# Kernel tuning notes

Measured on AMD Instinct MI355X. Metric: run time of the kernel, lower is better.

## Reference

```python
import jax, jax.numpy as jnp
import numpy as np

# Window-batch of 16x16 windows from a U-Net stage
B, C, H, W = 128, 128, 16, 16
HEADS = 8
EQK, EV = 128, 512      # embed_dim_qk, embed_dim_v (embed_dim=512, ratio=4)
L = H * W               # tokens per window (stride=1)


def _conv3x3(x, w, b):
    # NCHW 3x3 conv, padding 1
    out = jax.lax.conv_general_dilated(x, w, (1, 1), ((1, 1), (1, 1)),
                                       dimension_numbers=('NCHW', 'OIHW', 'NCHW'))
    return out + b[None, :, None, None]


def _pos_att(q, wq, bq, wk, bk, wv, bv, wo, bo, gamma):
    # MultiHeadAttention2D_POS, stride=1 -> conv_q/k/v are 1x1 convs
    hd, hdv = EQK // HEADS, EV // HEADS

    def proj(x, w, bias, d):
        y = jnp.einsum('bchw,ec->behw', x, w) + bias[None, :, None, None]
        return y.reshape(B, HEADS, d, L).transpose(0, 1, 3, 2)  # (B,h,L,d)

    pq = proj(q, wq, bq, hd)
    pk = proj(q, wk, bk, hd)
    pv = proj(q, wv, bv, hdv)
    attn = jax.nn.softmax(jnp.einsum('bhqd,bhkd->bhqk', pq, pk) * hd ** -0.5, axis=-1)
    out = jnp.einsum('bhqk,bhkd->bhqd', attn, pv)
    out = out.transpose(0, 1, 3, 2).reshape(B, EV, H, W)
    out = _conv3x3(out, wo, bo)             # proj_out: 3x3 conv EV->C
    return q + out * gamma                  # gamma-scaled residual


def _cha_att(q, wq, bq, wk, bk, wv, bv, wo, bo, gamma):
    # MultiHeadAttention2D_CHA: depthwise 1x1 grouped convs (channel multiplier = HEADS),
    # attention over the CHANNEL axis. Faithfully reproduces torch's reshape of the
    # group-major (c*HEADS+h) channel layout into (B, heads, C, L).
    def dwproj(x, w, bias):
        y = (x[:, :, None] * w.reshape(C, HEADS)[None, :, :, None, None]
             + bias.reshape(C, HEADS)[None, :, :, None, None])
        return y.reshape(B, C * HEADS, H, W).reshape(B, HEADS, C, L)

    pq = dwproj(q, wq, bq)
    pk = dwproj(q, wk, bk)
    pv = dwproj(q, wv, bv)
    attn = jax.nn.softmax(jnp.einsum('bhcl,bhdl->bhcd', pq, pk) * L ** -0.5, axis=-1)
    out = jnp.einsum('bhcd,bhdl->bhcl', attn, pv)      # (B,h,C,L)
    out = out.reshape(B, HEADS * C, H, W)
    # proj_out: grouped 1x1 ConvTranspose (== grouped 1x1 conv): sum each HEADS-sized group
    out = (out.reshape(B, C, HEADS, H, W)
           * wo.reshape(C, HEADS)[None, :, :, None, None]).sum(2) + bo[None, :, None, None]
    return q + out * gamma


def _forward(qkv_pos, qkv_cha,
             pos_wq, pos_bq, pos_wk, pos_bk, pos_wv, pos_bv, pos_wo, pos_bo, gamma_pos,
             cha_wq, cha_bq, cha_wk, cha_bk, cha_wv, cha_bv, cha_wo, cha_bo, gamma_cha,
             fuse_w, fuse_b):
    out_pos = _pos_att(qkv_pos, pos_wq, pos_bq, pos_wk, pos_bk, pos_wv, pos_bv,
                       pos_wo, pos_bo, gamma_pos)
    out_cha = _cha_att(qkv_cha, cha_wq, cha_bq, cha_wk, cha_bk, cha_wv, cha_bv,
                       cha_wo, cha_bo, gamma_cha)
    out = (out_pos + out_cha) * 0.5          # att_fusion='add' (slides=0 -> full slices)
    return _conv3x3(out, fuse_w, fuse_b)     # conv_out (Dropout2d is identity at eval)


def setup_inputs() -> dict:
    key = jax.random.key(0)
    ks = jax.random.split(key, 24)
    n = lambda k, shape, s=0.05: jax.random.normal(k, shape, dtype=jnp.float32) * s
    return {
        'qkv_pos': jax.random.normal(ks[0], (B, C, H, W), jnp.float32),
        'qkv_cha': jax.random.normal(ks[1], (B, C, H, W), jnp.float32),
        'pos_wq': n(ks[2], (EQK, C)), 'pos_bq': n(ks[3], (EQK,)),
        'pos_wk': n(ks[4], (EQK, C)), 'pos_bk': n(ks[5], (EQK,)),
        'pos_wv': n(ks[6], (EV, C)), 'pos_bv': n(ks[7], (EV,)),
        'pos_wo': n(ks[8], (C, EV, 3, 3)), 'pos_bo': n(ks[9], (C,)),
        'gamma_pos': jnp.array(0.1, jnp.float32),
        'cha_wq': n(ks[10], (C * HEADS,)), 'cha_bq': n(ks[11], (C * HEADS,)),
        'cha_wk': n(ks[12], (C * HEADS,)), 'cha_bk': n(ks[13], (C * HEADS,)),
        'cha_wv': n(ks[14], (C * HEADS,)), 'cha_bv': n(ks[15], (C * HEADS,)),
        'cha_wo': n(ks[16], (C * HEADS,)), 'cha_bo': n(ks[17], (C,)),
        'gamma_cha': jnp.array(0.1, jnp.float32),
        'fuse_w': n(ks[18], (C, C, 3, 3)), 'fuse_b': n(ks[19], (C,)),
    }


def reference(qkv_pos, qkv_cha,
              pos_wq, pos_bq, pos_wk, pos_bk, pos_wv, pos_bv, pos_wo, pos_bo, gamma_pos,
              cha_wq, cha_bq, cha_wk, cha_bk, cha_wv, cha_bv, cha_wo, cha_bo, gamma_cha,
              fuse_w, fuse_b):
    return _forward(qkv_pos, qkv_cha,
                    pos_wq, pos_bq, pos_wk, pos_bk, pos_wv, pos_bv, pos_wo, pos_bo, gamma_pos,
                    cha_wq, cha_bq, cha_wk, cha_bk, cha_wv, cha_bv, cha_wo, cha_bo, gamma_cha,
                    fuse_w, fuse_b)
```

## Files before the change

### kernel.cpp

```cpp
#include <hip/hip_runtime.h>
#include <cstdint>
#include <cstddef>

typedef unsigned short ushort_t;
typedef unsigned int uint_t;
typedef __attribute__((ext_vector_type(8))) short bf16x8;
typedef __attribute__((ext_vector_type(4))) float f32x4;

#define NB 128
#define NC 128
#define NL 256
#define NH 8
#define HD 16
#define HDV 64
#define NEV 512
#define PHALF 4194304

__device__ __forceinline__ ushort_t f2bf(float f) {
    uint_t u = __float_as_uint(f);
    u += 0x7fffu + ((u >> 16) & 1u);
    return (ushort_t)(u >> 16);
}
__device__ __forceinline__ float bf2f(ushort_t s) {
    return __uint_as_float(((uint_t)s) << 16);
}
__device__ __forceinline__ uint_t pack2(float lo, float hi) {
    return ((uint_t)f2bf(hi) << 16) | (uint_t)f2bf(lo);
}

template<int CIN>
__global__ __launch_bounds__(256) void k_wpack(const float* __restrict__ w,
                                               short* __restrict__ wp) {
    int idx = blockIdx.x * 256 + threadIdx.x;
    if (idx >= CIN * 1152) return;
    int j    = idx & 7;
    int lane = (idx >> 3) & 63;
    int frag = idx >> 9;
    int rt   = frag & 7;
    int tap  = (frag >> 3) % 9;
    int ch   = frag / 72;
    int co   = rt * 16 + (lane & 15);
    int g    = lane >> 4;
    int ci   = ch * 32 + g * 8 + j;
    wp[idx] = (short)f2bf(w[((size_t)co * CIN + ci) * 9 + tap]);
}

template<int E>
__global__ __launch_bounds__(256) void k_wpack_qkv(const float* __restrict__ w,
                                                   short* __restrict__ wp) {
    int idx = blockIdx.x * 256 + threadIdx.x;
    if (idx >= E * 128) return;
    int j    = idx & 7;
    int lane = (idx >> 3) & 63;
    int ch   = (idx >> 9) & 3;
    int rt   = idx >> 11;
    int n = lane & 15, g = lane >> 4;
    wp[idx] = (short)f2bf(w[(size_t)(rt*16 + n)*128 + ch*32 + g*8 + j]);
}

__global__ __launch_bounds__(256) void k_pos_mfma(
    const float* __restrict__ x,
    const short* __restrict__ wpq, const short* __restrict__ wpk,
    const short* __restrict__ wpv,
    const float* __restrict__ bq, const float* __restrict__ bk,
    const float* __restrict__ bv,
    ushort_t* __restrict__ att)
{
    const int h = blockIdx.x, b = blockIdx.y;
    const int t = threadIdx.x;
    const int lane = t & 63, w = t >> 6;
    const int n = lane & 15, g = lane >> 4;

    __shared__ __align__(16) short lds[31232];

    const f32x4 z4 = {0.f, 0.f, 0.f, 0.f};
    f32x4 qacc[4], kacc[4], vacc[16];
    #pragma unroll
    for (int ct = 0; ct < 4; ++ct) { qacc[ct] = z4; kacc[ct] = z4; }
    #pragma unroll
    for (int i = 0; i < 16; ++i) vacc[i] = z4;

    const float* xg = x + (size_t)b * NC * NL + t;

    #pragma unroll 1
    for (int ch = 0; ch < 4; ++ch) {
        __syncthreads();
        #pragma unroll
        for (int k8 = 0; k8 < 4; ++k8) {
            bf16x8 v8;
            #pragma unroll
            for (int jj = 0; jj < 8; ++jj)
                v8[jj] = (short)f2bf(xg[(ch*32 + k8*8 + jj) * NL]);
            *(bf16x8*)&lds[t*40 + k8*8] = v8;
        }
        __syncthreads();
        bf16x8 xb[4];
        #pragma unroll
        for (int ct = 0; ct < 4; ++ct)
            xb[ct] = *(const bf16x8*)&lds[(w*64 + ct*16 + n)*40 + g*8];
        const size_t fo = ((size_t)((h*4 + ch)*64) + lane) * 8;
        {
            bf16x8 aq = *(const bf16x8*)(wpq + fo);
            #pragma unroll
            for (int ct = 0; ct < 4; ++ct)
                qacc[ct] = __builtin_amdgcn_mfma_f32_16x16x32_bf16(aq, xb[ct], qacc[ct], 0, 0, 0);
        }
        {
            bf16x8 ak = *(const bf16x8*)(wpk + fo);
            #pragma unroll
            for (int ct = 0; ct < 4; ++ct)
                kacc[ct] = __builtin_amdgcn_mfma_f32_16x16x32_bf16(ak, xb[ct], kacc[ct], 0, 0, 0);
        }
        #pragma unroll
        for (int vt = 0; vt < 4; ++vt) {
            bf16x8 av = *(const bf16x8*)(wpv + ((size_t)((((h*4 + vt)*4) + ch)*64) + lane) * 8);
            #pragma unroll
            for (int ct = 0; ct < 4; ++ct)
                vacc[vt*4+ct] = __builtin_amdgcn_mfma_f32_16x16x32_bf16(av, xb[ct], vacc[vt*4+ct], 0, 0, 0);
        }
    }
    __syncthreads();

    {
        float bqv[4], bkv[4];
        #pragma unroll
        for (int r = 0; r < 4; ++r) {
            bqv[r] = bq[h*16 + g*4 + r];
            bkv[r] = bk[h*16 + g*4 + r];
        }
        #pragma unroll
        for (int ct = 0; ct < 4; ++ct) {
            uint2 qp, kp;
            qp.x = pack2(qacc[ct][0] + bqv[0], qacc[ct][1] + bqv[1]);
            qp.y = pack2(qacc[ct][2] + bqv[2], qacc[ct][3] + bqv[3]);
            *(uint2*)&lds[w*1024 + (ct*16 + n)*16 + g*4] = qp;
            kp.x = pack2(kacc[ct][0] + bkv[0], kacc[ct][1] + bkv[1]);
            kp.y = pack2(kacc[ct][2] + bkv[2], kacc[ct][3] + bkv[3]);
            *(uint2*)&lds[10240 + (w*64 + ct*16 + n)*16 + g*4] = kp;
        }
        #pragma unroll
        for (int vt = 0; vt < 4; ++vt) {
            float bv0 = bv[h*64 + vt*16 + g*4 + 0];
            float bv1 = bv[h*64 + vt*16 + g*4 + 1];
            float bv2 = bv[h*64 + vt*16 + g*4 + 2];
            float bv3 = bv[h*64 + vt*16 + g*4 + 3];
            #pragma unroll
            for (int ct = 0; ct < 4; ++ct) {
                const int col = w*64 + ct*16 + n;
                lds[14336 + (vt*16 + g*4 + 0)*264 + col] = (short)f2bf(vacc[vt*4+ct][0] + bv0);
                lds[14336 + (vt*16 + g*4 + 1)*264 + col] = (short)f2bf(vacc[vt*4+ct][1] + bv1);
                lds[14336 + (vt*16 + g*4 + 2)*264 + col] = (short)f2bf(vacc[vt*4+ct][2] + bv2);
                lds[14336 + (vt*16 + g*4 + 3)*264 + col] = (short)f2bf(vacc[vt*4+ct][3] + bv3);
            }
        }
    }
    __syncthreads();

    #pragma unroll 1
    for (int qt = 0; qt < 4; ++qt) {
        bf16x8 qf = (bf16x8){0,0,0,0,0,0,0,0};
        if (g < 2) qf = *(const bf16x8*)&lds[w*1024 + (qt*16 + n)*16 + g*8];
        f32x4 s[16];
        #pragma unroll
        for (int kt = 0; kt < 16; ++kt) {
            bf16x8 kf = (bf16x8){0,0,0,0,0,0,0,0};
            if (g < 2) kf = *(const bf16x8*)&lds[10240 + (kt*16 + n)*16 + g*8];
            s[kt] = __builtin_amdgcn_mfma_f32_16x16x32_bf16(kf, qf, z4, 0, 0, 0);
        }
        float m = -3.0e38f;
        #pragma unroll
        for (int kt = 0; kt < 16; ++kt)
            #pragma unroll
            for (int r = 0; r < 4; ++r)
                m = fmaxf(m, s[kt][r]);
        m = fmaxf(m, __shfl_xor(m, 16));
        m = fmaxf(m, __shfl_xor(m, 32));
        float den = 0.f;
        #pragma unroll
        for (int kt = 0; kt < 16; ++kt)
            #pragma unroll
            for (int r = 0; r < 4; ++r) {
                float e = __expf((s[kt][r] - m) * 0.25f);
                s[kt][r] = e;
                den += e;
            }
        den += __shfl_xor(den, 16);
        den += __shfl_xor(den, 32);
        const float inv = 1.f / den;

        f32x4 oacc[4] = {z4, z4, z4, z4};
        #pragma unroll
        for (int c2 = 0; c2 < 8; ++c2) {
            #pragma unroll
            for (int u = 0; u < 2; ++u) {
                const int kt = 2*c2 + u;
                uint2 pp;
                pp.x = pack2(s[kt][0], s[kt][1]);
                pp.y = pack2(s[kt][2], s[kt][3]);
                *(uint2*)&lds[4096 + w*640 + n*40 + u*16 + g*4] = pp;
            }
            bf16x8 pf = *(const bf16x8*)&lds[4096 + w*640 + n*40 + g*8];
            #pragma unroll
            for (int vt = 0; vt < 4; ++vt) {
                bf16x8 av = *(const bf16x8*)&lds[14336 + (vt*16 + n)*264 + c2*32 + g*8];
                oacc[vt] = __builtin_amdgcn_mfma_f32_16x16x32_bf16(av, pf, oacc[vt], 0, 0, 0);
            }
        }
        ushort_t* ap = att + (((size_t)b*NL + (w*64 + qt*16 + n))*NEV + h*HDV + g*4);
        #pragma unroll
        for (int vt = 0; vt < 4; ++vt) {
            uint2 op;
            op.x = pack2(oacc[vt][0]*inv, oacc[vt][1]*inv);
            op.y = pack2(oacc[vt][2]*inv, oacc[vt][3]*inv);
            *(uint2*)(ap + vt*16) = op;
        }
    }
}

__global__ __launch_bounds__(512, 2) void k_conv_ci(
    const ushort_t* __restrict__ att, const short* __restrict__ wp,
    ushort_t* __restrict__ P)
{
    const int kc = blockIdx.x, b = blockIdx.y;
    const int t = threadIdx.x;
    const int lane = t & 63, w = t >> 6;
    const int wr = w >> 2, wc = w & 3;
    const int n = lane & 15, gl = lane >> 4;

    __shared__ __align__(16) short ims[2][10368];

    {
        bf16x8 z = {0,0,0,0,0,0,0,0};
        bf16x8* p = (bf16x8*)&ims[0][0];
        for (int i = t; i < 2592; i += 512) p[i] = z;
    }

    f32x4 acc[4][4];
    #pragma unroll
    for (int i = 0; i < 4; ++i)
        #pragma unroll
        for (int j = 0; j < 4; ++j) acc[i][j] = (f32x4){0.f,0.f,0.f,0.f};

    const int g1 = t & 3, x1 = (t >> 2) & 15, y1 = t >> 6;
    const ushort_t* src1 = att + ((size_t)(b*NL + y1*16 + x1))*NEV + kc*256 + g1*8;
    const ushort_t* src2 = att + ((size_t)(b*NL + (y1+8)*16 + x1))*NEV + kc*256 + g1*8;
    const int slot1 = (((y1+1)*4 + g1)*18 + x1 + 1) * 8;
    const int slot2 = (((y1+9)*4 + g1)*18 + x1 + 1) * 8;

    bf16x8 v1 = *(const bf16x8*)src1;
    bf16x8 v2 = *(const bf16x8*)src2;
    __syncthreads();

    #pragma unroll 1
    for (int ch = 0; ch < 8; ++ch) {
        short* buf = &ims[ch & 1][0];
        *(bf16x8*)&buf[slot1] = v1;
        *(bf16x8*)&buf[slot2] = v2;
        if (ch < 7) {
            v1 = *(const bf16x8*)(src1 + (ch + 1) * 32);
            v2 = *(const bf16x8*)(src2 + (ch + 1) * 32);
        }
        __syncthreads();
        #pragma unroll
        for (int tap = 0; tap < 9; ++tap) {
            const int dy = tap / 3, dx = tap % 3;
            bf16x8 Bf[4];
            #pragma unroll
            for (int ct = 0; ct < 4; ++ct)
                Bf[ct] = *(const bf16x8*)&buf[((((wc*4 + ct + dy)*4) + gl)*18 + n + dx) * 8];
            bf16x8 Af[4];
            #pragma unroll
            for (int rt = 0; rt < 4; ++rt)
                Af[rt] = *(const bf16x8*)(wp +
                    ((size_t)(((kc*8 + ch)*9 + tap)*8 + wr*4 + rt)) * 512 + lane*8);
            #pragma unroll
            for (int rt = 0; rt < 4; ++rt)
                #pragma unroll
                for (int ct = 0; ct < 4; ++ct)
                    acc[rt][ct] = __builtin_amdgcn_mfma_f32_16x16x32_bf16(
                        Af[rt], Bf[ct], acc[rt][ct], 0, 0, 0);
        }
    }

    ushort_t* Pb = P + (size_t)kc * PHALF + (size_t)b * NL * NC;
    #pragma unroll
    for (int rt = 0; rt < 4; ++rt) {
        const int co0 = wr*64 + rt*16 + gl*4;
        #pragma unroll
        for (int ct = 0; ct < 4; ++ct) {
            const int l = wc*64 + ct*16 + n;
            uint2 u;
            u.x = pack2(acc[rt][ct][0], acc[rt][ct][1]);
            u.y = pack2(acc[rt][ct][2], acc[rt][ct][3]);
            *(uint2*)(Pb + (size_t)l*NC + co0) = u;
        }
    }
}

__global__ __launch_bounds__(512, 2) void k_conv_co(
    const float* __restrict__ comb, const short* __restrict__ wp,
    const float* __restrict__ bias, float* __restrict__ out)
{
    const int kc = blockIdx.x, b = blockIdx.y;
    const int t = threadIdx.x;
    const int lane = t & 63, w = t >> 6;
    const int wr = w & 1, wc = w >> 1;
    const int n = lane & 15, gl = lane >> 4;

    __shared__ __align__(16) short ims[2][10368];

    {
        bf16x8 z = {0,0,0,0,0,0,0,0};
        bf16x8* p = (bf16x8*)&ims[0][0];
        for (int i = t; i < 2592; i += 512) p[i] = z;
    }

    f32x4 acc[2][4];
    #pragma unroll
    for (int i = 0; i < 2; ++i)
        #pragma unroll
        for (int j = 0; j < 4; ++j) acc[i][j] = (f32x4){0.f,0.f,0.f,0.f};

    const int g1 = t & 3, x1 = (t >> 2) & 15, y1 = t >> 6;
    const float* s1 = comb + ((size_t)(b*NL + y1*16 + x1))*NC + g1*8;
    const float* s2 = comb + ((size_t)(b*NL + (y1+8)*16 + x1))*NC + g1*8;
    const int slot1 = (((y1+1)*4 + g1)*18 + x1 + 1) * 8;
    const int slot2 = (((y1+9)*4 + g1)*18 + x1 + 1) * 8;

    float4 a1 = *(const float4*)s1,       b1_ = *(const float4*)(s1 + 4);
    float4 a2 = *(const float4*)s2,       b2_ = *(const float4*)(s2 + 4);
    __syncthreads();

    #pragma unroll 1
    for (int ch = 0; ch < 4; ++ch) {
        short* buf = &ims[ch & 1][0];
        bf16x8 w1, w2;
        w1[0]=(short)f2bf(a1.x);  w1[1]=(short)f2bf(a1.y);
        w1[2]=(short)f2bf(a1.z);  w1[3]=(short)f2bf(a1.w);
        w1[4]=(short)f2bf(b1_.x); w1[5]=(short)f2bf(b1_.y);
        w1[6]=(short)f2bf(b1_.z); w1[7]=(short)f2bf(b1_.w);
        w2[0]=(short)f2bf(a2.x);  w2[1]=(short)f2bf(a2.y);
        w2[2]=(short)f2bf(a2.z);  w2[3]=(short)f2bf(a2.w);
        w2[4]=(short)f2bf(b2_.x); w2[5]=(short)f2bf(b2_.y);
        w2[6]=(short)f2bf(b2_.z); w2[7]=(short)f2bf(b2_.w);
        *(bf16x8*)&buf[slot1] = w1;
        *(bf16x8*)&buf[slot2] = w2;
        if (ch < 3) {
            a1  = *(const float4*)(s1 + (ch+1)*32);
            b1_ = *(const float4*)(s1 + (ch+1)*32 + 4);
            a2  = *(const float4*)(s2 + (ch+1)*32);
            b2_ = *(const float4*)(s2 + (ch+1)*32 + 4);
        }
        __syncthreads();
        #pragma unroll
        for (int tap = 0; tap < 9; ++tap) {
            const int dy = tap / 3, dx = tap % 3;
            bf16x8 Bf[4];
            #pragma unroll
            for (int ct = 0; ct < 4; ++ct)
                Bf[ct] = *(const bf16x8*)&buf[((((wc*4 + ct + dy)*4) + gl)*18 + n + dx) * 8];
            bf16x8 Af[2];
            #pragma unroll
            for (int rt = 0; rt < 2; ++rt)
                Af[rt] = *(const bf16x8*)(wp +
                    ((size_t)((ch*9 + tap)*8 + kc*4 + wr*2 + rt)) * 512 + lane*8);
            #pragma unroll
            for (int rt = 0; rt < 2; ++rt)
                #pragma unroll
                for (int ct = 0; ct < 4; ++ct)
                    acc[rt][ct] = __builtin_amdgcn_mfma_f32_16x16x32_bf16(
                        Af[rt], Bf[ct], acc[rt][ct], 0, 0, 0);
        }
    }

    #pragma unroll
    for (int rt = 0; rt < 2; ++rt) {
        const int co0 = kc*64 + wr*32 + rt*16 + gl*4;
        const float c0 = bias[co0+0], c1 = bias[co0+1],
                    c2 = bias[co0+2], c3 = bias[co0+3];
        #pragma unroll
        for (int ct = 0; ct < 4; ++ct) {
            const int l = wc*64 + ct*16 + n;
            f32x4 a = acc[rt][ct];
            out[((size_t)b*NC + co0+0)*NL + l] = c0 + a[0];
            out[((size_t)b*NC + co0+1)*NL + l] = c1 + a[1];
            out[((size_t)b*NC + co0+2)*NL + l] = c2 + a[2];
            out[((size_t)b*NC + co0+3)*NL + l] = c3 + a[3];
        }
    }
}

#define NLP 260
__global__ __launch_bounds__(256) void k_cha(
    const float* __restrict__ xc,
    const float* __restrict__ cwq, const float* __restrict__ cbq,
    const float* __restrict__ cwk, const float* __restrict__ cbk,
    const float* __restrict__ cwv, const float* __restrict__ cbv,
    const float* __restrict__ cwo, const float* __restrict__ cbo,
    const float* __restrict__ gamma,
    const ushort_t* __restrict__ P, const float* __restrict__ qpos,
    const float* __restrict__ pbo, const float* __restrict__ gpos,
    float* __restrict__ comb)
{
    const int h = blockIdx.x, b = blockIdx.y, t = threadIdx.x;
    __shared__ float qh[16][NLP];
    __shared__ float G_s[16][17];
    __shared__ float S_s[16];
    __shared__ float wq_s[128], bq_s[128], wk_s[128], bk_s[128], wv_s[128], bv_s[128];
    __shared__ float A_s[128][17];
    __shared__ float B_s[128];
    __shared__ float M_s[16][17];
    __shared__ float c_s[16];

    #pragma unroll
    for (int j = 0; j < 16; ++j)
        qh[j][t] = xc[((size_t)b*NC + h*16 + j)*NL + t];
    if (t < 128) {
        const int k = h*128 + t;
        wq_s[t] = cwq[k]; bq_s[t] = cbq[k];
        wk_s[t] = cwk[k]; bk_s[t] = cbk[k];
        wv_s[t] = cwv[k]; bv_s[t] = cbv[k];
    }
    __syncthreads();
    {
        const int i = t >> 4, j = t & 15;
        const float4* qi = (const float4*)qh[i];
        const float4* qj = (const float4*)qh[j];
        float gg = 0.f;
        for (int l4 = 0; l4 < NL/4; ++l4) {
            float4 a = qi[l4], c = qj[l4];
            gg = fmaf(a.x,c.x,fmaf(a.y,c.y,fmaf(a.z,c.z,fmaf(a.w,c.w,gg))));
        }
        G_s[i][j] = gg;
    }
    if (t < 16) {
        const float4* qi = (const float4*)qh[t];
        float s = 0.f;
        for (int l4 = 0; l4 < NL/4; ++l4) { float4 a = qi[l4]; s += a.x + a.y + a.z + a.w; }
        S_s[t] = s;
    }
    __syncthreads();
    if (t < 128) {
        const int c2 = t, cg = c2 >> 3;
        const float wqc = wq_s[c2], bqc = bq_s[c2];
        float Pv[16];
        #pragma unroll
        for (int j = 0; j < 16; ++j) Pv[j] = wqc*G_s[cg][j] + bqc*S_s[j];
        const float Qc = wqc*S_s[cg] + bqc*256.0f;
        float mx = -3.0e38f;
        #pragma unroll
        for (int dg = 0; dg < 16; ++dg) {
            #pragma unroll
            for (int dj = 0; dj < 8; ++dj) {
                const int d = dg*8 + dj;
                float s = wk_s[d]*Pv[dg] + bk_s[d]*Qc;
                mx = fmaxf(mx, s);
            }
        }
        float A[16];
        #pragma unroll
        for (int j = 0; j < 16; ++j) A[j] = 0.f;
        float Bv = 0.f, den = 0.f;
        #pragma unroll
        for (int dg = 0; dg < 16; ++dg) {
            #pragma unroll
            for (int dj = 0; dj < 8; ++dj) {
                const int d = dg*8 + dj;
                float s = wk_s[d]*Pv[dg] + bk_s[d]*Qc;
                float e = __expf((s - mx) * 0.0625f);
                den += e;
                A[dg] = fmaf(e, wv_s[d], A[dg]);
                Bv = fmaf(e, bv_s[d], Bv);
            }
        }
        const float inv = 1.f / den;
        #pragma unroll
        for (int j = 0; j < 16; ++j) A_s[c2][j] = A[j]*inv;
        B_s[c2] = Bv*inv;
    }
    __syncthreads();
    {
        const int cl = t >> 4, j = t & 15;
        const int cp = h*16 + cl;
        float m = 0.f;
        #pragma unroll
        for (int hp = 0; hp < 8; ++hp)
            m = fmaf(cwo[cp*8+hp], A_s[cl*8+hp][j], m);
        M_s[cl][j] = m;
        if (j == 0) {
            float cc = cbo[cp];
            #pragma unroll
            for (int hp = 0; hp < 8; ++hp)
                cc = fmaf(cwo[cp*8+hp], B_s[cl*8+hp], cc);
            c_s[cl] = cc;
        }
    }
    __syncthreads();
    {
        const float g  = gamma[0];
        const float gp = gpos[0];
        const int l = t;
        float av[16];
        #pragma unroll
        for (int cl = 0; cl < 16; ++cl) {
            float a = c_s[cl];
            #pragma unroll
            for (int j = 0; j < 16; ++j)
                a = fmaf(M_s[cl][j], qh[j][l], a);
            av[cl] = a;
        }
        const ushort_t* p0 = P + ((size_t)b*NL + l)*NC + h*16;
        const ushort_t* p1 = p0 + PHALF;
        const float* qp = qpos + ((size_t)b*NC + h*16)*NL + l;
        float4* cp4 = (float4*)(comb + ((size_t)b*NL + l)*NC + h*16);
        #pragma unroll
        for (int q = 0; q < 4; ++q) {
            uint2 u0 = *(const uint2*)(p0 + 4*q);
            uint2 u1 = *(const uint2*)(p1 + 4*q);
            float s0 = bf2f((ushort_t)(u0.x & 0xffffu)) + bf2f((ushort_t)(u1.x & 0xffffu));
            float s1 = bf2f((ushort_t)(u0.x >> 16))     + bf2f((ushort_t)(u1.x >> 16));
            float s2 = bf2f((ushort_t)(u0.y & 0xffffu)) + bf2f((ushort_t)(u1.y & 0xffffu));
            float s3 = bf2f((ushort_t)(u0.y >> 16))     + bf2f((ushort_t)(u1.y >> 16));
            float4 c;
            c.x = 0.5f*(qp[(4*q+0)*NL] + gp*(pbo[h*16+4*q+0] + s0) + qh[4*q+0][l] + g*av[4*q+0]);
            c.y = 0.5f*(qp[(4*q+1)*NL] + gp*(pbo[h*16+4*q+1] + s1) + qh[4*q+1][l] + g*av[4*q+1]);
            c.z = 0.5f*(qp[(4*q+2)*NL] + gp*(pbo[h*16+4*q+2] + s2) + qh[4*q+2][l] + g*av[4*q+2]);
            c.w = 0.5f*(qp[(4*q+3)*NL] + gp*(pbo[h*16+4*q+3] + s3) + qh[4*q+3][l] + g*av[4*q+3]);
            cp4[q] = c;
        }
    }
}

extern "C" void kernel_launch(void* const* d_in, const int* in_sizes, int n_in,
                              void* d_out, int out_size, void* d_ws, size_t ws_size,
                              hipStream_t stream)
{
    const float* qpos = (const float*)d_in[0];
    const float* qcha = (const float*)d_in[1];
    const float* pwq  = (const float*)d_in[2];
    const float* pbq  = (const float*)d_in[3];
    const float* pwk  = (const float*)d_in[4];
    const float* pbk  = (const float*)d_in[5];
    const float* pwv  = (const float*)d_in[6];
    const float* pbv  = (const float*)d_in[7];
    const float* pwo  = (const float*)d_in[8];
    const float* pbo  = (const float*)d_in[9];
    const float* gpos = (const float*)d_in[10];
    const float* cwq  = (const float*)d_in[11];
    const float* cbq  = (const float*)d_in[12];
    const float* cwk  = (const float*)d_in[13];
    const float* cbk  = (const float*)d_in[14];
    const float* cwv  = (const float*)d_in[15];
    const float* cbv  = (const float*)d_in[16];
    const float* cwo  = (const float*)d_in[17];
    const float* cbo  = (const float*)d_in[18];
    const float* gcha = (const float*)d_in[19];
    const float* fw   = (const float*)d_in[20];
    const float* fb   = (const float*)d_in[21];
    float* outp = (float*)d_out;

    char* ws = (char*)d_ws;
    ushort_t* att  = (ushort_t*)ws;
    float*    comb = (float*)ws;
    ushort_t* P    = (ushort_t*)(ws + 33554432);
    short*    wp1  = (short*)(ws + 50331648);
    short*    wp2  = (short*)(ws + 51511296);
    short*    wpq  = (short*)(ws + 51806208);
    short*    wpk  = (short*)(ws + 51838976);
    short*    wpv  = (short*)(ws + 51871744);

    k_wpack<NEV><<<dim3((NEV*1152 + 255)/256), 256, 0, stream>>>(pwo, wp1);
    k_wpack<NC ><<<dim3((NC *1152 + 255)/256), 256, 0, stream>>>(fw,  wp2);
    k_wpack_qkv<128><<<dim3(64),  256, 0, stream>>>(pwq, wpq);
    k_wpack_qkv<128><<<dim3(64),  256, 0, stream>>>(pwk, wpk);
    k_wpack_qkv<512><<<dim3(256), 256, 0, stream>>>(pwv, wpv);

    k_pos_mfma<<<dim3(NH, NB), 256, 0, stream>>>(qpos, wpq, wpk, wpv,
                                                 pbq, pbk, pbv, att);
    k_conv_ci<<<dim3(2, NB), 512, 0, stream>>>(att, wp1, P);
    k_cha<<<dim3(NH, NB), 256, 0, stream>>>(qcha, cwq, cbq, cwk, cbk, cwv, cbv,
                                            cwo, cbo, gcha,
                                            P, qpos, pbo, gpos, comb);
    k_conv_co<<<dim3(2, NB), 512, 0, stream>>>(comb, wp2, fb, outp);
}
```

Measured before the change: 185.9 us.

## Pre-transpose input to bf16 token-major once, drop per-head LDS staging

Adds a kernel that converts the fp32 NCHW input into a bf16 token-major buffer once per batch, instead of every one of the 8 head blocks reconverting and staging it through LDS with barriers. The QKV projection now loads MFMA operands straight from global memory. The V MFMA operand order is swapped so each V result can be written to LDS as packed 4-element stores rather than scalar stores. This costs an extra launch and a 8 MB round trip through a workspace region that is reused later by P, but removes redundant fp32 reads, conversions and the LDS footprint and syncs in the projection loop.

```diff
diff --git a/kernel.cpp b/kernel.cpp
--- a/kernel.cpp
+++ b/kernel.cpp
@@ -58,8 +58,22 @@
     wp[idx] = (short)f2bf(w[(size_t)(rt*16 + n)*128 + ch*32 + g*8 + j]);
 }
 
+__global__ __launch_bounds__(256) void k_xpose(const float* __restrict__ x,
+                                               ushort_t* __restrict__ xbf) {
+    const int half = blockIdx.x, b = blockIdx.y, t = threadIdx.x;
+    const float* src = x + (size_t)b*NC*NL + (size_t)half*64*NL + t;
+    ushort_t* dst = xbf + ((size_t)b*NL + t)*NC + half*64;
+    #pragma unroll
+    for (int k8 = 0; k8 < 8; ++k8) {
+        bf16x8 v;
+        #pragma unroll
+        for (int j = 0; j < 8; ++j) v[j] = (short)f2bf(src[(k8*8 + j)*NL]);
+        *(bf16x8*)(dst + k8*8) = v;
+    }
+}
+
 __global__ __launch_bounds__(256) void k_pos_mfma(
-    const float* __restrict__ x,
+    const ushort_t* __restrict__ xbf,
     const short* __restrict__ wpq, const short* __restrict__ wpk,
     const short* __restrict__ wpv,
     const float* __restrict__ bq, const float* __restrict__ bk,
@@ -71,33 +85,25 @@
     const int lane = t & 63, w = t >> 6;
     const int n = lane & 15, g = lane >> 4;
 
-    __shared__ __align__(16) short lds[31232];
+    __shared__ __align__(16) short lds[27648];
 
     const f32x4 z4 = {0.f, 0.f, 0.f, 0.f};
-    f32x4 qacc[4], kacc[4], vacc[16];
+    f32x4 qacc[4], kacc[4], vacc[4][4];
     #pragma unroll
     for (int ct = 0; ct < 4; ++ct) { qacc[ct] = z4; kacc[ct] = z4; }
     #pragma unroll
-    for (int i = 0; i < 16; ++i) vacc[i] = z4;
-
-    const float* xg = x + (size_t)b * NC * NL + t;
-
-    #pragma unroll 1
+    for (int vt = 0; vt < 4; ++vt)
+        #pragma unroll
+        for (int ct = 0; ct < 4; ++ct) vacc[vt][ct] = z4;
+
+    const ushort_t* xr = xbf + ((size_t)(b*NL + w*64 + n))*NC;
+
+    #pragma unroll 2
     for (int ch = 0; ch < 4; ++ch) {
-        __syncthreads();
-        #pragma unroll
-        for (int k8 = 0; k8 < 4; ++k8) {
-            bf16x8 v8;
-            #pragma unroll
-            for (int jj = 0; jj < 8; ++jj)
-                v8[jj] = (short)f2bf(xg[(ch*32 + k8*8 + jj) * NL]);
-            *(bf16x8*)&lds[t*40 + k8*8] = v8;
-        }
-        __syncthreads();
         bf16x8 xb[4];
         #pragma unroll
         for (int ct = 0; ct < 4; ++ct)
-            xb[ct] = *(const bf16x8*)&lds[(w*64 + ct*16 + n)*40 + g*8];
+            xb[ct] = *(const bf16x8*)(xr + ct*16*NC + ch*32 + g*8);
         const size_t fo = ((size_t)((h*4 + ch)*64) + lane) * 8;
         {
             bf16x8 aq = *(const bf16x8*)(wpq + fo);
@@ -116,10 +122,9 @@
             bf16x8 av = *(const bf16x8*)(wpv + ((size_t)((((h*4 + vt)*4) + ch)*64) + lane) * 8);
             #pragma unroll
             for (int ct = 0; ct < 4; ++ct)
-                vacc[vt*4+ct] = __builtin_amdgcn_mfma_f32_16x16x32_bf16(av, xb[ct], vacc[vt*4+ct], 0, 0, 0);
-        }
-    }
-    __syncthreads();
+                vacc[vt][ct] = __builtin_amdgcn_mfma_f32_16x16x32_bf16(xb[ct], av, vacc[vt][ct], 0, 0, 0);
+        }
+    }
 
     {
         float bqv[4], bkv[4];
@@ -133,24 +138,20 @@
             uint2 qp, kp;
             qp.x = pack2(qacc[ct][0] + bqv[0], qacc[ct][1] + bqv[1]);
             qp.y = pack2(qacc[ct][2] + bqv[2], qacc[ct][3] + bqv[3]);
-            *(uint2*)&lds[w*1024 + (ct*16 + n)*16 + g*4] = qp;
+            *(uint2*)&lds[4096 + w*1024 + (ct*16 + n)*16 + g*4] = qp;
             kp.x = pack2(kacc[ct][0] + bkv[0], kacc[ct][1] + bkv[1]);
             kp.y = pack2(kacc[ct][2] + bkv[2], kacc[ct][3] + bkv[3]);
-            *(uint2*)&lds[10240 + (w*64 + ct*16 + n)*16 + g*4] = kp;
+            *(uint2*)&lds[(w*64 + ct*16 + n)*16 + g*4] = kp;
         }
         #pragma unroll
         for (int vt = 0; vt < 4; ++vt) {
-            float bv0 = bv[h*64 + vt*16 + g*4 + 0];
-            float bv1 = bv[h*64 + vt*16 + g*4 + 1];
-            float bv2 = bv[h*64 + vt*16 + g*4 + 2];
-            float bv3 = bv[h*64 + vt*16 + g*4 + 3];
+            const float bvv = bv[h*64 + vt*16 + n];
             #pragma unroll
             for (int ct = 0; ct < 4; ++ct) {
-                const int col = w*64 + ct*16 + n;
-                lds[14336 + (vt*16 + g*4 + 0)*264 + col] = (short)f2bf(vacc[vt*4+ct][0] + bv0);
-                lds[14336 + (vt*16 + g*4 + 1)*264 + col] = (short)f2bf(vacc[vt*4+ct][1] + bv1);
-                lds[14336 + (vt*16 + g*4 + 2)*264 + col] = (short)f2bf(vacc[vt*4+ct][2] + bv2);
-                lds[14336 + (vt*16 + g*4 + 3)*264 + col] = (short)f2bf(vacc[vt*4+ct][3] + bv3);
+                uint2 vp;
+                vp.x = pack2(vacc[vt][ct][0] + bvv, vacc[vt][ct][1] + bvv);
+                vp.y = pack2(vacc[vt][ct][2] + bvv, vacc[vt][ct][3] + bvv);
+                *(uint2*)&lds[10752 + (vt*16 + n)*264 + w*64 + ct*16 + g*4] = vp;
             }
         }
     }
@@ -159,12 +160,12 @@
     #pragma unroll 1
     for (int qt = 0; qt < 4; ++qt) {
         bf16x8 qf = (bf16x8){0,0,0,0,0,0,0,0};
-        if (g < 2) qf = *(const bf16x8*)&lds[w*1024 + (qt*16 + n)*16 + g*8];
+        if (g < 2) qf = *(const bf16x8*)&lds[4096 + w*1024 + (qt*16 + n)*16 + g*8];
         f32x4 s[16];
         #pragma unroll
         for (int kt = 0; kt < 16; ++kt) {
             bf16x8 kf = (bf16x8){0,0,0,0,0,0,0,0};
-            if (g < 2) kf = *(const bf16x8*)&lds[10240 + (kt*16 + n)*16 + g*8];
+            if (g < 2) kf = *(const bf16x8*)&lds[(kt*16 + n)*16 + g*8];
             s[kt] = __builtin_amdgcn_mfma_f32_16x16x32_bf16(kf, qf, z4, 0, 0, 0);
         }
         float m = -3.0e38f;
@@ -197,12 +198,12 @@
                 uint2 pp;
                 pp.x = pack2(s[kt][0], s[kt][1]);
                 pp.y = pack2(s[kt][2], s[kt][3]);
-                *(uint2*)&lds[4096 + w*640 + n*40 + u*16 + g*4] = pp;
+                *(uint2*)&lds[8192 + w*640 + n*40 + u*16 + g*4] = pp;
             }
-            bf16x8 pf = *(const bf16x8*)&lds[4096 + w*640 + n*40 + g*8];
+            bf16x8 pf = *(const bf16x8*)&lds[8192 + w*640 + n*40 + g*8];
             #pragma unroll
             for (int vt = 0; vt < 4; ++vt) {
-                bf16x8 av = *(const bf16x8*)&lds[14336 + (vt*16 + n)*264 + c2*32 + g*8];
+                bf16x8 av = *(const bf16x8*)&lds[10752 + (vt*16 + n)*264 + c2*32 + g*8];
                 oacc[vt] = __builtin_amdgcn_mfma_f32_16x16x32_bf16(av, pf, oacc[vt], 0, 0, 0);
             }
         }
@@ -563,6 +564,7 @@
     ushort_t* att  = (ushort_t*)ws;
     float*    comb = (float*)ws;
     ushort_t* P    = (ushort_t*)(ws + 33554432);
+    ushort_t* xbf  = (ushort_t*)(ws + 33554432);
     short*    wp1  = (short*)(ws + 50331648);
     short*    wp2  = (short*)(ws + 51511296);
     short*    wpq  = (short*)(ws + 51806208);
@@ -575,7 +577,8 @@
     k_wpack_qkv<128><<<dim3(64),  256, 0, stream>>>(pwk, wpk);
     k_wpack_qkv<512><<<dim3(256), 256, 0, stream>>>(pwv, wpv);
 
-    k_pos_mfma<<<dim3(NH, NB), 256, 0, stream>>>(qpos, wpq, wpk, wpv,
+    k_xpose<<<dim3(2, NB), 256, 0, stream>>>(qpos, xbf);
+    k_pos_mfma<<<dim3(NH, NB), 256, 0, stream>>>(xbf, wpq, wpk, wpv,
                                                  pbq, pbk, pbv, att);
     k_conv_ci<<<dim3(2, NB), 512, 0, stream>>>(att, wp1, P);
     k_cha<<<dim3(NH, NB), 256, 0, stream>>>(qcha, cwq, cbq, cwk, cbk, cwv, cbv,
```

New measurement: 182.9 us. No clear change (-1.6%).
